# Optimization experiments

Hardware: AMD Instinct MI355X
Metric: run time of the kernel (lower is better)

The kernel has to match this reference:

```python
import jax, jax.numpy as jnp
import numpy as np

B, N_MAX, D_MODEL, K_F, ROD_ID_DIM = 16384, 64, 256, 8, 8
BETA = 10000.0
PRECOMP = 64  # FourierFeatures precompute_limit
DISK_FEAT = 2 + 2 * K_F + 3 + ROD_ID_DIM   # 29
ROD_FEAT = 2 + 1 + 1 + 2 * 2 * K_F + ROD_ID_DIM  # 44


def fourier_table():
    # sin/cos interleaved as in torch: stack([sin,cos],-1).view(P, 2K)
    k = jnp.arange(K_F, dtype=jnp.float32)
    omega = BETA ** (-2.0 * k / (2.0 * K_F))
    idx = jnp.arange(PRECOMP, dtype=jnp.float32)
    oi = idx[:, None] * omega  # (P, K)
    return jnp.stack([jnp.sin(oi), jnp.cos(oi)], axis=-1).reshape(PRECOMP, 2 * K_F)


def setup_inputs() -> dict:
    key = jax.random.key(0)
    ks = jax.random.split(key, 8)
    state = jax.random.randint(ks[0], (B, N_MAX), 0, 3, dtype=jnp.int32)
    s = 0.02
    return {
        'state': state,
        'rod_id_embed': jax.random.normal(ks[1], (3, ROD_ID_DIM), jnp.float32),
        'disk_W': jax.random.normal(ks[2], (DISK_FEAT, D_MODEL), jnp.float32) * s,
        'disk_b': jax.random.normal(ks[3], (D_MODEL,), jnp.float32) * s,
        'rod_W': jax.random.normal(ks[4], (ROD_FEAT, D_MODEL), jnp.float32) * s,
        'rod_b': jax.random.normal(ks[5], (D_MODEL,), jnp.float32) * s,
        'null_fourier': jax.random.normal(ks[6], (2 * K_F,), jnp.float32) * s,
        'padding_embedding': jax.random.normal(ks[7], (D_MODEL,), jnp.float32) * s,
    }


def reference(state, rod_id_embed, disk_W, disk_b, rod_W, rod_b, null_fourier, padding_embedding):
    Bq, N = state.shape
    table = fourier_table()                      # (P, 2K)
    valid = state != -1                          # (B, N)
    lengths = valid.sum(axis=1)                  # (B,)
    state_safe = jnp.clip(state, 0, 2)

    # ---- vectorized _compute_state_info ----
    onehot = (state[:, None, :] == jnp.arange(3, dtype=state.dtype)[None, :, None]) & valid[:, None, :]  # (B,3,N)
    oh = onehot.astype(jnp.float32)
    counts = oh.sum(-1)                          # (B,3) disks per rod
    is_empty = counts == 0.0
    len_norm = counts / jnp.maximum(lengths, 1).astype(jnp.float32)[:, None]
    top_disk = jnp.argmax(onehot, axis=-1)       # min index on rod (top = smallest disk)
    bottom_disk = (N - 1) - jnp.argmax(onehot[:, :, ::-1], axis=-1)
    # per-disk: 'above' = # of smaller-index disks on same rod (exclusive prefix sum)
    cum = jnp.cumsum(oh, axis=-1) - oh           # (B,3,N)
    above = jnp.take_along_axis(cum, state_safe[:, None, :], axis=1)[:, 0, :]   # (B,N)
    height = jnp.take_along_axis(counts, state_safe, axis=1)                    # (B,N)
    vf = valid.astype(jnp.float32)
    is_top = (above == 0.0).astype(jnp.float32) * vf
    is_bottom = (above == height - 1.0).astype(jnp.float32) * vf
    depth_norm = jnp.where(height > 1.0, above / jnp.maximum(height - 1.0, 1.0), 0.0) * vf

    # ---- rod nodes (3) ----
    rod_type = jnp.broadcast_to(jnp.array([0.0, 1.0], jnp.float32), (Bq, 3, 2))
    top_f = table[top_disk]                      # (B,3,2K)
    bot_f = table[bottom_disk]
    emp = is_empty[:, :, None]
    top_f = jnp.where(emp, null_fourier, top_f)
    bot_f = jnp.where(emp, null_fourier, bot_f)
    rod_ids = jnp.broadcast_to(rod_id_embed[None], (Bq, 3, ROD_ID_DIM))
    rod_feats = jnp.concatenate([
        rod_type, len_norm[:, :, None], emp.astype(jnp.float32), top_f, bot_f, rod_ids], axis=-1)  # (B,3,44)
    rod_emb = jnp.einsum('brf,fd->brd', rod_feats, rod_W) + rod_b

    # ---- disk nodes (N) ----
    disk_type = jnp.broadcast_to(jnp.array([1.0, 0.0], jnp.float32), (Bq, N, 2))
    size_f = jnp.broadcast_to(table[:N][None], (Bq, N, 2 * K_F))
    rod_id_vec = rod_id_embed[state_safe]        # (B,N,rod_id_dim)
    disk_feats = jnp.concatenate([
        disk_type, size_f, depth_norm[:, :, None], is_top[:, :, None], is_bottom[:, :, None], rod_id_vec], axis=-1)  # (B,N,29)
    disk_emb = jnp.einsum('bnf,fd->bnd', disk_feats, disk_W) + disk_b
    disk_emb = jnp.where(valid[:, :, None], disk_emb, padding_embedding)

    return jnp.concatenate([rod_emb, disk_emb], axis=1)  # (B, 3+N, d_model)
```

## Files before the change

### kernel.cpp

```cpp
#include <hip/hip_runtime.h>

#define DM 256
#define NMAX 64

#define OFF_RIDPROJ 16384
#define OFF_BASEROD 17152
#define OFF_RODTOP  17920
#define OFF_RODBOT  34560

typedef float vf4 __attribute__((ext_vector_type(4)));

static __device__ __forceinline__ vf4 ld4(const float* p) {
  return *reinterpret_cast<const vf4*>(p);
}
static __device__ __forceinline__ void st4_nt(float* p, vf4 v) {
  __builtin_nontemporal_store(v, reinterpret_cast<vf4*>(p));
}

__global__ void precomp_kernel(
    const float* __restrict__ rod_id_embed,
    const float* __restrict__ disk_W,
    const float* __restrict__ disk_b,
    const float* __restrict__ rod_W,
    const float* __restrict__ rod_b,
    const float* __restrict__ null_fourier,
    float* __restrict__ ws) {
  const int idx = blockIdx.x;
  const int d = threadIdx.x;

  float F[16];
  if (idx < 64) {
#pragma unroll
    for (int k = 0; k < 8; ++k) {
      float omega = powf(10000.0f, -(float)k * 0.125f);
      float a = (float)idx * omega;
      F[2 * k]     = sinf(a);
      F[2 * k + 1] = cosf(a);
    }
  } else {
#pragma unroll
    for (int k = 0; k < 16; ++k) F[k] = null_fourier[k];
  }

  float* baseDisk = ws;
  float* ridproj  = ws + OFF_RIDPROJ;
  float* baseRod  = ws + OFF_BASEROD;
  float* rodTop   = ws + OFF_RODTOP;
  float* rodBot   = ws + OFF_RODBOT;

  float t = 0.f, bo = 0.f;
#pragma unroll
  for (int k = 0; k < 16; ++k) {
    t  += F[k] * rod_W[(4 + k) * DM + d];
    bo += F[k] * rod_W[(20 + k) * DM + d];
  }
  rodTop[idx * DM + d] = t;
  rodBot[idx * DM + d] = bo;

  if (idx < 64) {
    float base = disk_b[d] + disk_W[0 * DM + d];
#pragma unroll
    for (int k = 0; k < 16; ++k) base += F[k] * disk_W[(2 + k) * DM + d];
    baseDisk[(size_t)idx * DM + d] = base;
  }
  if (idx < 3) {
    float rp = 0.f;
    float br = rod_b[d] + rod_W[1 * DM + d];
#pragma unroll
    for (int j = 0; j < 8; ++j) {
      rp += rod_id_embed[idx * 8 + j] * disk_W[(21 + j) * DM + d];
      br += rod_id_embed[idx * 8 + j] * rod_W[(36 + j) * DM + d];
    }
    ridproj[idx * DM + d] = rp;
    baseRod[idx * DM + d] = br;
  }
}

__launch_bounds__(256)
__global__ void enc_kernel(
    const int* __restrict__ state,
    const float* __restrict__ disk_W,
    const float* __restrict__ rod_W,
    const float* __restrict__ padding_embedding,
    const float* __restrict__ ws,
    float* __restrict__ out) {
  const float* baseDisk = ws;
  const float* ridproj  = ws + OFF_RIDPROJ;
  const float* baseRod  = ws + OFF_BASEROD;
  const float* rodTop   = ws + OFF_RODTOP;
  const float* rodBot   = ws + OFF_RODBOT;

  const int tid  = threadIdx.x;
  const int q    = tid >> 6;
  const int lane = tid & 63;
  const long b   = blockIdx.x;

  const int s = state[b * NMAX + lane];
  const bool valid = (s >= 0);
  const int ss = s <= 0 ? 0 : (s >= 2 ? 2 : s);
  const unsigned long long m0 = __ballot(valid && s == 0);
  const unsigned long long m1 = __ballot(valid && s == 1);
  const unsigned long long m2 = __ballot(valid && s == 2);
  const unsigned long long vm = __ballot(valid);
  const unsigned long long mym = (ss == 0) ? m0 : ((ss == 1) ? m1 : m2);
  const int above  = __popcll(mym & ((1ull << lane) - 1ull));
  const int height = __popcll(mym);

  const float depf = (valid && height > 1) ? (float)above / (float)(height - 1) : 0.f;
  const int flags = valid ? ((ss + 1) | (above == 0 ? 4 : 0) |
                             (above == height - 1 ? 8 : 0))
                          : 0;

  const unsigned long long mr = (lane == 0) ? m0 : ((lane == 1) ? m1 : m2);
  const int cnt = __popcll(mr);
  const int lengths = __popcll(vm);
  const float lnf = (float)cnt / (float)(lengths > 1 ? lengths : 1);
  const int ti = cnt ? (int)__builtin_ctzll(mr) : 64;
  const int bi = cnt ? 63 - (int)__builtin_clzll(mr) : 64;
  const int rodpack = ti | (bi << 8) | ((cnt == 0) ? 0x10000 : 0);

  const int c0 = lane * 4;
  const vf4 Wdep = ld4(disk_W + 18 * DM + c0);
  const vf4 Wt   = ld4(disk_W + 19 * DM + c0);
  const vf4 Wb   = ld4(disk_W + 20 * DM + c0);
  const vf4 pad  = ld4(padding_embedding + c0);
  const vf4 rp0  = ld4(ridproj + 0 * DM + c0);
  const vf4 rp1  = ld4(ridproj + 1 * DM + c0);
  const vf4 rp2  = ld4(ridproj + 2 * DM + c0);

  float* outB = out + (size_t)b * 67 * DM;

  if (q < 3) {
    const vf4 rW2 = ld4(rod_W + 2 * DM + c0);
    const vf4 rW3 = ld4(rod_W + 3 * DM + c0);
    const float ln = __uint_as_float(
        __builtin_amdgcn_readlane(__float_as_uint(lnf), q));
    const int rpk = __builtin_amdgcn_readlane(rodpack, q);
    const int rti = rpk & 0xff;
    const int rbi = (rpk >> 8) & 0xff;
    const float em = (float)((rpk >> 16) & 1);
    vf4 v = ld4(baseRod + q * DM + c0);
    v += ld4(rodTop + (size_t)rti * DM + c0);
    v += ld4(rodBot + (size_t)rbi * DM + c0);
    v += ln * rW2 + em * rW3;
    st4_nt(outB + q * DM + c0, v);
  }

#pragma unroll 4
  for (int r = q + 4; r < 67; r += 4) {
    const int i = r - 3;
    const int fl = __builtin_amdgcn_readlane(flags, i);
    const float dep = __uint_as_float(
        __builtin_amdgcn_readlane(__float_as_uint(depf), i));
    vf4 v;
    if (fl) {
      const vf4 base = ld4(baseDisk + (size_t)i * DM + c0);
      const int code = fl & 3;
      const vf4 rp = (code == 1) ? rp0 : ((code == 2) ? rp1 : rp2);
      const float tt = (float)((fl >> 2) & 1);
      const float bb = (float)((fl >> 3) & 1);
      v = base + rp + dep * Wdep + tt * Wt + bb * Wb;
    } else {
      v = pad;
    }
    st4_nt(outB + (size_t)r * DM + c0, v);
  }

  if (q == 3) {
    const int i = 0;
    const int fl = __builtin_amdgcn_readlane(flags, i);
    const float dep = __uint_as_float(
        __builtin_amdgcn_readlane(__float_as_uint(depf), i));
    vf4 v;
    if (fl) {
      const vf4 base = ld4(baseDisk + (size_t)i * DM + c0);
      const int code = fl & 3;
      const vf4 rp = (code == 1) ? rp0 : ((code == 2) ? rp1 : rp2);
      const float tt = (float)((fl >> 2) & 1);
      const float bb = (float)((fl >> 3) & 1);
      v = base + rp + dep * Wdep + tt * Wt + bb * Wb;
    } else {
      v = pad;
    }
    st4_nt(outB + 3 * DM + c0, v);
  }
}

extern "C" void kernel_launch(void* const* d_in, const int* in_sizes, int n_in,
                              void* d_out, int out_size, void* d_ws, size_t ws_size,
                              hipStream_t stream) {
  const int*   state             = (const int*)d_in[0];
  const float* rod_id_embed      = (const float*)d_in[1];
  const float* disk_W            = (const float*)d_in[2];
  const float* disk_b            = (const float*)d_in[3];
  const float* rod_W             = (const float*)d_in[4];
  const float* rod_b             = (const float*)d_in[5];
  const float* null_fourier      = (const float*)d_in[6];
  const float* padding_embedding = (const float*)d_in[7];
  float* ws  = (float*)d_ws;
  float* out = (float*)d_out;

  const int B = in_sizes[0] / NMAX;

  hipLaunchKernelGGL(precomp_kernel, dim3(65), dim3(256), 0, stream,
                     rod_id_embed, disk_W, disk_b, rod_W, rod_b, null_fourier, ws);
  hipLaunchKernelGGL(enc_kernel, dim3(B), dim3(256), 0, stream,
                     state, disk_W, rod_W, padding_embedding, ws, out);
}
```

Measured before the change: 223.6 us.

## Process eight batch rows per workgroup with XCD-aware block remapping

The encoder kernel now launches one workgroup per eight batch rows instead of one per row. Weight vectors and the per-rod base row are loaded once and reused across the eight rows. Block IDs are remapped so consecutive rows land on the same XCD, keeping each workgroup's output region contiguous. This cuts launch and setup overhead for a store-bound kernel but leaves fewer workgroups to hide memory latency.

```diff
diff --git a/kernel.cpp b/kernel.cpp
--- a/kernel.cpp
+++ b/kernel.cpp
@@ -76,6 +76,8 @@
   }
 }
 
+#define BPB 8
+
 __launch_bounds__(256)
 __global__ void enc_kernel(
     const int* __restrict__ state,
@@ -83,7 +85,8 @@
     const float* __restrict__ rod_W,
     const float* __restrict__ padding_embedding,
     const float* __restrict__ ws,
-    float* __restrict__ out) {
+    float* __restrict__ out,
+    int Btot) {
   const float* baseDisk = ws;
   const float* ridproj  = ws + OFF_RIDPROJ;
   const float* baseRod  = ws + OFF_BASEROD;
@@ -93,31 +96,10 @@
   const int tid  = threadIdx.x;
   const int q    = tid >> 6;
   const int lane = tid & 63;
-  const long b   = blockIdx.x;
-
-  const int s = state[b * NMAX + lane];
-  const bool valid = (s >= 0);
-  const int ss = s <= 0 ? 0 : (s >= 2 ? 2 : s);
-  const unsigned long long m0 = __ballot(valid && s == 0);
-  const unsigned long long m1 = __ballot(valid && s == 1);
-  const unsigned long long m2 = __ballot(valid && s == 2);
-  const unsigned long long vm = __ballot(valid);
-  const unsigned long long mym = (ss == 0) ? m0 : ((ss == 1) ? m1 : m2);
-  const int above  = __popcll(mym & ((1ull << lane) - 1ull));
-  const int height = __popcll(mym);
-
-  const float depf = (valid && height > 1) ? (float)above / (float)(height - 1) : 0.f;
-  const int flags = valid ? ((ss + 1) | (above == 0 ? 4 : 0) |
-                             (above == height - 1 ? 8 : 0))
-                          : 0;
-
-  const unsigned long long mr = (lane == 0) ? m0 : ((lane == 1) ? m1 : m2);
-  const int cnt = __popcll(mr);
-  const int lengths = __popcll(vm);
-  const float lnf = (float)cnt / (float)(lengths > 1 ? lengths : 1);
-  const int ti = cnt ? (int)__builtin_ctzll(mr) : 64;
-  const int bi = cnt ? 63 - (int)__builtin_clzll(mr) : 64;
-  const int rodpack = ti | (bi << 8) | ((cnt == 0) ? 0x10000 : 0);
+
+  const int nwg  = gridDim.x;
+  const int bid  = blockIdx.x;
+  const int wgid = (bid & 7) * (nwg >> 3) + (bid >> 3);
 
   const int c0 = lane * 4;
   const vf4 Wdep = ld4(disk_W + 18 * DM + c0);
@@ -127,62 +109,90 @@
   const vf4 rp0  = ld4(ridproj + 0 * DM + c0);
   const vf4 rp1  = ld4(ridproj + 1 * DM + c0);
   const vf4 rp2  = ld4(ridproj + 2 * DM + c0);
-
-  float* outB = out + (size_t)b * 67 * DM;
-
-  if (q < 3) {
-    const vf4 rW2 = ld4(rod_W + 2 * DM + c0);
-    const vf4 rW3 = ld4(rod_W + 3 * DM + c0);
-    const float ln = __uint_as_float(
-        __builtin_amdgcn_readlane(__float_as_uint(lnf), q));
-    const int rpk = __builtin_amdgcn_readlane(rodpack, q);
-    const int rti = rpk & 0xff;
-    const int rbi = (rpk >> 8) & 0xff;
-    const float em = (float)((rpk >> 16) & 1);
-    vf4 v = ld4(baseRod + q * DM + c0);
-    v += ld4(rodTop + (size_t)rti * DM + c0);
-    v += ld4(rodBot + (size_t)rbi * DM + c0);
-    v += ln * rW2 + em * rW3;
-    st4_nt(outB + q * DM + c0, v);
-  }
+  const vf4 rW2  = ld4(rod_W + 2 * DM + c0);
+  const vf4 rW3  = ld4(rod_W + 3 * DM + c0);
+  const vf4 bR   = (q < 3) ? ld4(baseRod + q * DM + c0) : pad;
+
+  for (int bb = 0; bb < BPB; ++bb) {
+    const long b = (long)wgid * BPB + bb;
+    if (b >= Btot) break;
+
+    const int s = state[b * NMAX + lane];
+    const bool valid = (s >= 0);
+    const int ss = s <= 0 ? 0 : (s >= 2 ? 2 : s);
+    const unsigned long long m0 = __ballot(valid && s == 0);
+    const unsigned long long m1 = __ballot(valid && s == 1);
+    const unsigned long long m2 = __ballot(valid && s == 2);
+    const unsigned long long vm = __ballot(valid);
+    const unsigned long long mym = (ss == 0) ? m0 : ((ss == 1) ? m1 : m2);
+    const int above  = __popcll(mym & ((1ull << lane) - 1ull));
+    const int height = __popcll(mym);
+
+    const float depf =
+        (valid && height > 1) ? (float)above / (float)(height - 1) : 0.f;
+    const int flags = valid ? ((ss + 1) | (above == 0 ? 4 : 0) |
+                               (above == height - 1 ? 8 : 0))
+                            : 0;
+
+    const unsigned long long mr = (lane == 0) ? m0 : ((lane == 1) ? m1 : m2);
+    const int cnt = __popcll(mr);
+    const int lengths = __popcll(vm);
+    const float lnf = (float)cnt / (float)(lengths > 1 ? lengths : 1);
+    const int ti = cnt ? (int)__builtin_ctzll(mr) : 64;
+    const int bi = cnt ? 63 - (int)__builtin_clzll(mr) : 64;
+    const int rodpack = ti | (bi << 8) | ((cnt == 0) ? 0x10000 : 0);
+
+    float* outB = out + (size_t)b * 67 * DM;
+
+    if (q < 3) {
+      const float ln = __uint_as_float(
+          __builtin_amdgcn_readlane(__float_as_uint(lnf), q));
+      const int rpk = __builtin_amdgcn_readlane(rodpack, q);
+      const int rti = rpk & 0xff;
+      const int rbi = (rpk >> 8) & 0xff;
+      const float em = (float)((rpk >> 16) & 1);
+      vf4 v = bR;
+      v += ld4(rodTop + (size_t)rti * DM + c0);
+      v += ld4(rodBot + (size_t)rbi * DM + c0);
+      v += ln * rW2 + em * rW3;
+      st4_nt(outB + q * DM + c0, v);
+    } else {
+      const int fl = __builtin_amdgcn_readlane(flags, 0);
+      const float dep = __uint_as_float(
+          __builtin_amdgcn_readlane(__float_as_uint(depf), 0));
+      vf4 v;
+      if (fl) {
+        const vf4 base = ld4(baseDisk + c0);
+        const int code = fl & 3;
+        const vf4 rp = (code == 1) ? rp0 : ((code == 2) ? rp1 : rp2);
+        const float tt = (float)((fl >> 2) & 1);
+        const float bb2 = (float)((fl >> 3) & 1);
+        v = base + rp + dep * Wdep + tt * Wt + bb2 * Wb;
+      } else {
+        v = pad;
+      }
+      st4_nt(outB + 3 * DM + c0, v);
+    }
 
 #pragma unroll 4
-  for (int r = q + 4; r < 67; r += 4) {
-    const int i = r - 3;
-    const int fl = __builtin_amdgcn_readlane(flags, i);
-    const float dep = __uint_as_float(
-        __builtin_amdgcn_readlane(__float_as_uint(depf), i));
-    vf4 v;
-    if (fl) {
-      const vf4 base = ld4(baseDisk + (size_t)i * DM + c0);
-      const int code = fl & 3;
-      const vf4 rp = (code == 1) ? rp0 : ((code == 2) ? rp1 : rp2);
-      const float tt = (float)((fl >> 2) & 1);
-      const float bb = (float)((fl >> 3) & 1);
-      v = base + rp + dep * Wdep + tt * Wt + bb * Wb;
-    } else {
-      v = pad;
-    }
-    st4_nt(outB + (size_t)r * DM + c0, v);
-  }
-
-  if (q == 3) {
-    const int i = 0;
-    const int fl = __builtin_amdgcn_readlane(flags, i);
-    const float dep = __uint_as_float(
-        __builtin_amdgcn_readlane(__float_as_uint(depf), i));
-    vf4 v;
-    if (fl) {
-      const vf4 base = ld4(baseDisk + (size_t)i * DM + c0);
-      const int code = fl & 3;
-      const vf4 rp = (code == 1) ? rp0 : ((code == 2) ? rp1 : rp2);
-      const float tt = (float)((fl >> 2) & 1);
-      const float bb = (float)((fl >> 3) & 1);
-      v = base + rp + dep * Wdep + tt * Wt + bb * Wb;
-    } else {
-      v = pad;
-    }
-    st4_nt(outB + 3 * DM + c0, v);
+    for (int r = q + 4; r < 67; r += 4) {
+      const int i = r - 3;
+      const int fl = __builtin_amdgcn_readlane(flags, i);
+      const float dep = __uint_as_float(
+          __builtin_amdgcn_readlane(__float_as_uint(depf), i));
+      vf4 v;
+      if (fl) {
+        const vf4 base = ld4(baseDisk + (size_t)i * DM + c0);
+        const int code = fl & 3;
+        const vf4 rp = (code == 1) ? rp0 : ((code == 2) ? rp1 : rp2);
+        const float tt = (float)((fl >> 2) & 1);
+        const float bb2 = (float)((fl >> 3) & 1);
+        v = base + rp + dep * Wdep + tt * Wt + bb2 * Wb;
+      } else {
+        v = pad;
+      }
+      st4_nt(outB + (size_t)r * DM + c0, v);
+    }
   }
 }
 
@@ -202,8 +212,11 @@
 
   const int B = in_sizes[0] / NMAX;
 
+  int nwg = (B + BPB - 1) / BPB;
+  nwg = (nwg + 7) & ~7;
+
   hipLaunchKernelGGL(precomp_kernel, dim3(65), dim3(256), 0, stream,
                      rod_id_embed, disk_W, disk_b, rod_W, rod_b, null_fourier, ws);
-  hipLaunchKernelGGL(enc_kernel, dim3(B), dim3(256), 0, stream,
-                     state, disk_W, rod_W, padding_embedding, ws, out);
-}
+  hipLaunchKernelGGL(enc_kernel, dim3(nwg), dim3(256), 0, stream,
+                     state, disk_W, rod_W, padding_embedding, ws, out, B);
+}
```

Measured after the change: 233.9 us. 4.6% more time.
